# Performance work log

Hardware: AMD Instinct MI355X
Metric: run time of the kernel (lower is better)

The kernel has to match this reference:

```python
import jax, jax.numpy as jnp
import numpy as np


def setup_inputs() -> dict:
    key = jax.random.key(0)
    k1, k2, k3 = jax.random.split(key, 3)
    N, E, D_IN, D_OUT = 100000, 3200000, 256, 256
    x = jax.random.normal(k1, (N, D_IN), dtype=jnp.float32)
    W = jax.random.normal(k2, (D_OUT, D_IN), dtype=jnp.float32) * (1.0 / np.sqrt(D_IN))
    edge_index = jax.random.randint(k3, (2, E), 0, N, dtype=jnp.int32)
    return {"x": x, "W": W, "edge_index": edge_index}


def reference(x, W, edge_index):
    N = x.shape[0]
    # add self loops (static shape: E + N edges)
    loops = jnp.arange(N, dtype=edge_index.dtype)
    src = jnp.concatenate([edge_index[0], loops])  # [E+N]
    dst = jnp.concatenate([edge_index[1], loops])  # [E+N]
    # symmetric degree normalization: deg = bincount over source index
    deg = jax.ops.segment_sum(jnp.ones_like(src, dtype=x.dtype), src, num_segments=N)
    deg_rsqrt = jax.lax.rsqrt(deg)
    vals = deg_rsqrt[src] * deg_rsqrt[dst]  # [E+N]
    # dense projection then SpMM: out[i] = sum_e A[src_e=i] * h[dst_e]
    h = x @ W.T  # [N, D_OUT]
    msgs = vals[:, None] * h[dst]  # gather + scale
    out = jax.ops.segment_sum(msgs, src, num_segments=N)  # scatter-add
    return out
```

## Files before the change

kernel.cpp:

```cpp
#include <hip/hip_runtime.h>
#include <hip/hip_bf16.h>
#include <stdint.h>

#define D 256
#define NBUCK 391
#define BSHIFT 8
#define TILE 4096

typedef short short8 __attribute__((ext_vector_type(8)));
typedef float f32x4 __attribute__((ext_vector_type(4)));
typedef unsigned int u32x2 __attribute__((ext_vector_type(2)));

__device__ __forceinline__ float bf2f(unsigned short u) {
  return __uint_as_float(((unsigned)u) << 16);
}
__device__ __forceinline__ unsigned short f2bf(float f) {
  unsigned u = __float_as_uint(f);
  unsigned r = u + 0x7FFFu + ((u >> 16) & 1u);
  return (unsigned short)(r >> 16);
}

__global__ void bucket_hist_kernel(const int* __restrict__ src, int* __restrict__ bcount, int E) {
  __shared__ int h[NBUCK];
  for (int i = threadIdx.x; i < NBUCK; i += 256) h[i] = 0;
  __syncthreads();
  int gid = blockIdx.x * 256 + threadIdx.x;
  for (int e = gid; e < E; e += 256 * 256) atomicAdd(&h[src[e] >> BSHIFT], 1);
  __syncthreads();
  for (int i = threadIdx.x; i < NBUCK; i += 256) {
    int c = h[i];
    if (c) atomicAdd(&bcount[i], c);
  }
}

__global__ void bucket_scan_kernel(const int* __restrict__ bcount, int* __restrict__ bbase,
                                   int* __restrict__ gcursor) {
  __shared__ int sc[2][512];
  int tid = threadIdx.x;
  sc[0][tid] = (tid < NBUCK) ? bcount[tid] : 0;
  __syncthreads();
  int d = 0;
  for (int off = 1; off < 512; off <<= 1) {
    int v = sc[d][tid];
    if (tid >= off) v += sc[d][tid - off];
    sc[d ^ 1][tid] = v;
    __syncthreads();
    d ^= 1;
  }
  if (tid < NBUCK) {
    int excl = (tid == 0) ? 0 : sc[d][tid - 1];
    bbase[tid] = excl;
    gcursor[tid] = excl;
  }
}

__launch_bounds__(256)
__global__ void binscatter_kernel(const int* __restrict__ src, const int* __restrict__ dst,
                                  int* __restrict__ gcursor, int* __restrict__ ebuf, int E) {
  __shared__ int hist[NBUCK];
  __shared__ int lstart[512];
  __shared__ int gbase[NBUCK];
  __shared__ int sc[2][512];
  __shared__ int stag[TILE];
  __shared__ unsigned short sbuck[TILE];

  int tid = threadIdx.x;
  int base = blockIdx.x * TILE;
  int tilecount = E - base;
  if (tilecount > TILE) tilecount = TILE;

  for (int i = tid; i < NBUCK; i += 256) hist[i] = 0;
  __syncthreads();

  int esrc[16], edst[16];
#pragma unroll
  for (int k = 0; k < 16; k++) {
    int e = base + k * 256 + tid;
    if (e < E) {
      esrc[k] = src[e];
      edst[k] = dst[e];
      atomicAdd(&hist[esrc[k] >> BSHIFT], 1);
    } else {
      esrc[k] = -1;
      edst[k] = 0;
    }
  }
  __syncthreads();

  for (int i = tid; i < 512; i += 256) sc[0][i] = (i < NBUCK) ? hist[i] : 0;
  __syncthreads();
  int d = 0;
  for (int off = 1; off < 512; off <<= 1) {
    for (int i = tid; i < 512; i += 256) {
      int v = sc[d][i];
      if (i >= off) v += sc[d][i - off];
      sc[d ^ 1][i] = v;
    }
    __syncthreads();
    d ^= 1;
  }
  for (int i = tid; i < 512; i += 256) lstart[i] = (i == 0) ? 0 : sc[d][i - 1];
  __syncthreads();

  for (int b = tid; b < NBUCK; b += 256) {
    int c = hist[b];
    if (c) gbase[b] = atomicAdd(&gcursor[b], c);
  }
  __syncthreads();

  for (int i = tid; i < NBUCK; i += 256) hist[i] = 0;
  __syncthreads();

#pragma unroll
  for (int k = 0; k < 16; k++) {
    if (esrc[k] >= 0) {
      int b = esrc[k] >> BSHIFT;
      int r = atomicAdd(&hist[b], 1);
      int pos = lstart[b] + r;
      stag[pos] = edst[k] | ((esrc[k] & 255) << 20);
      sbuck[pos] = (unsigned short)b;
    }
  }
  __syncthreads();

  for (int s = tid; s < tilecount; s += 256) {
    int b = sbuck[s];
    ebuf[gbase[b] + (s - lstart[b])] = stag[s];
  }
}

__launch_bounds__(256)
__global__ void bucketsort_kernel(const int* __restrict__ ebuf, const int* __restrict__ bbase,
                                  const int* __restrict__ bcount, int* __restrict__ csr,
                                  int2* __restrict__ meta, float* __restrict__ rnorm, int N) {
  __shared__ int ncnt[256];
  __shared__ int nstart[256];
  __shared__ int sc[2][256];
  int tid = threadIdx.x;
  int b = blockIdx.x;
  int base = bbase[b];
  int cnt = bcount[b];
  int node0 = b << BSHIFT;

  ncnt[tid] = 0;
  __syncthreads();
  for (int s = tid; s < cnt; s += 256) {
    int v = ebuf[base + s];
    atomicAdd(&ncnt[v >> 20], 1);
  }
  __syncthreads();

  int mycnt = ncnt[tid];
  sc[0][tid] = mycnt;
  __syncthreads();
  int d = 0;
  for (int off = 1; off < 256; off <<= 1) {
    int v = sc[d][tid];
    if (tid >= off) v += sc[d][tid - off];
    sc[d ^ 1][tid] = v;
    __syncthreads();
    d ^= 1;
  }
  nstart[tid] = (tid == 0) ? 0 : sc[d][tid - 1];
  __syncthreads();

  int node = node0 + tid;
  if (node < N) {
    meta[node] = make_int2(base + nstart[tid], mycnt);
    rnorm[node] = rsqrtf((float)(mycnt + 1));
  }

  ncnt[tid] = 0;
  __syncthreads();
  for (int s = tid; s < cnt; s += 256) {
    int v = ebuf[base + s];
    int nl = v >> 20;
    int r = atomicAdd(&ncnt[nl], 1);
    csr[base + nstart[nl] + r] = v & 0xFFFFF;
  }
}

__global__ void convx_kernel(const float* __restrict__ x, unsigned short* __restrict__ xb,
                             int n, int npad) {
  int i4 = blockIdx.x * 256 + threadIdx.x;
  long long elem = (long long)i4 * 4;
  if (elem >= (long long)npad * D) return;
  int row = (int)(elem / D);
  ushort4 o;
  if (row < n) {
    const float4 v = *(const float4*)&x[elem];
    o.x = f2bf(v.x); o.y = f2bf(v.y); o.z = f2bf(v.z); o.w = f2bf(v.w);
  } else {
    o = make_ushort4(0, 0, 0, 0);
  }
  *(ushort4*)&xb[elem] = o;
}

__global__ void convw_kernel(const float* __restrict__ w, unsigned short* __restrict__ wb) {
  int i4 = blockIdx.x * 256 + threadIdx.x;
  int elem = i4 * 4;
  const float4 v = *(const float4*)&w[elem];
  ushort4 o;
  o.x = f2bf(v.x); o.y = f2bf(v.y); o.z = f2bf(v.z); o.w = f2bf(v.w);
  *(ushort4*)&wb[elem] = o;
}

__launch_bounds__(256)
__global__ void gemm_kernel(const unsigned short* __restrict__ A,
                            const unsigned short* __restrict__ B,
                            unsigned short* __restrict__ Hout,
                            const float* __restrict__ rnorm, int n) {
  __shared__ unsigned short sA[128 * 32];
  __shared__ unsigned short sB[128 * 32];
  int tid = threadIdx.x;
  int wave = tid >> 6, lane = tid & 63;
  int wm = wave >> 1, wn = wave & 1;
  int l16 = lane & 15, quad = lane >> 4;
  int arow0 = blockIdx.x * 128;
  int brow0 = blockIdx.y * 128;

  f32x4 acc[4][4];
  const f32x4 zero = {0.f, 0.f, 0.f, 0.f};
#pragma unroll
  for (int i = 0; i < 4; i++)
#pragma unroll
    for (int j = 0; j < 4; j++) acc[i][j] = zero;

  for (int k0 = 0; k0 < 256; k0 += 32) {
#pragma unroll
    for (int it = 0; it < 2; ++it) {
      int c = it * 256 + tid;
      int row = c >> 2, cc = (c & 3) * 8;
      *(int4*)&sA[c * 8] = *(const int4*)&A[(arow0 + row) * 256 + k0 + cc];
      *(int4*)&sB[c * 8] = *(const int4*)&B[(brow0 + row) * 256 + k0 + cc];
    }
    __syncthreads();
    short8 af[4], bfr[4];
#pragma unroll
    for (int i = 0; i < 4; i++)
      af[i] = *(const short8*)&sA[(wm * 64 + i * 16 + l16) * 32 + quad * 8];
#pragma unroll
    for (int j = 0; j < 4; j++)
      bfr[j] = *(const short8*)&sB[(wn * 64 + j * 16 + l16) * 32 + quad * 8];
#pragma unroll
    for (int i = 0; i < 4; i++)
#pragma unroll
      for (int j = 0; j < 4; j++)
        acc[i][j] = __builtin_amdgcn_mfma_f32_16x16x32_bf16(af[i], bfr[j], acc[i][j], 0, 0, 0);
    __syncthreads();
  }

#pragma unroll
  for (int i = 0; i < 4; i++) {
    int rowb = arow0 + wm * 64 + i * 16 + quad * 4;
#pragma unroll
    for (int r = 0; r < 4; r++) {
      int gr = rowb + r;
      float rn = (gr < n) ? rnorm[gr] : 0.f;
#pragma unroll
      for (int j = 0; j < 4; j++) {
        int col = brow0 + wn * 64 + j * 16 + l16;
        Hout[(size_t)gr * 256 + col] = f2bf(acc[i][j][r] * rn);
      }
    }
  }
}

__launch_bounds__(256)
__global__ void gather_kernel(const unsigned short* __restrict__ hs,
                              const int2* __restrict__ meta,
                              const float* __restrict__ rnorm,
                              const int* __restrict__ csr,
                              float* __restrict__ out, int n) {
  const int wave = threadIdx.x >> 6;
  const int lane = threadIdx.x & 63;
  const int node = blockIdx.x * 4 + wave;
  if (node >= n) return;
  long long mm = __builtin_nontemporal_load((const long long*)&meta[node]);
  const int start = (int)mm;
  const int cnt = (int)(mm >> 32);
  const int loff = lane << 2;

  float a0 = 0.f, a1 = 0.f, a2 = 0.f, a3 = 0.f;

#define GRP16(G)                                                          \
  {                                                                       \
    u32x2 v[16];                                                          \
    _Pragma("unroll")                                                     \
    for (int u = 0; u < 16; ++u) {                                        \
      int r = __builtin_amdgcn_readlane(idxv, (G) + u);                   \
      v[u] = *(const u32x2*)&hs[((size_t)r << 8) + loff];                 \
    }                                                                     \
    _Pragma("unroll")                                                     \
    for (int u = 0; u < 16; ++u) {                                        \
      a0 += bf2f((unsigned short)v[u][0]);                                \
      a1 += bf2f((unsigned short)(v[u][0] >> 16));                        \
      a2 += bf2f((unsigned short)v[u][1]);                                \
      a3 += bf2f((unsigned short)(v[u][1] >> 16));                        \
    }                                                                     \
  }

  int idxv = __builtin_nontemporal_load(&csr[start + lane]);
  int base = 0;
  while (base + 64 <= cnt) {
    int idxn = __builtin_nontemporal_load(&csr[start + base + 64 + lane]);
    GRP16(0) GRP16(16) GRP16(32) GRP16(48)
    idxv = idxn;
    base += 64;
  }
  int m = cnt - base;
  int g = 0;
  for (; g + 16 <= m; g += 16) GRP16(g)
  for (; g < m; ++g) {
    int r = __builtin_amdgcn_readlane(idxv, g);
    u32x2 v = *(const u32x2*)&hs[((size_t)r << 8) + loff];
    a0 += bf2f((unsigned short)v[0]);
    a1 += bf2f((unsigned short)(v[0] >> 16));
    a2 += bf2f((unsigned short)v[1]);
    a3 += bf2f((unsigned short)(v[1] >> 16));
  }
#undef GRP16

  u32x2 us = *(const u32x2*)&hs[((size_t)node << 8) + loff];
  float rn = __builtin_nontemporal_load(&rnorm[node]);
  f32x4 o;
  o[0] = rn * (a0 + bf2f((unsigned short)us[0]));
  o[1] = rn * (a1 + bf2f((unsigned short)(us[0] >> 16)));
  o[2] = rn * (a2 + bf2f((unsigned short)us[1]));
  o[3] = rn * (a3 + bf2f((unsigned short)(us[1] >> 16)));
  __builtin_nontemporal_store(o, (f32x4*)&out[(size_t)node * 256 + loff]);
}

extern "C" void kernel_launch(void* const* d_in, const int* in_sizes, int n_in,
                              void* d_out, int out_size, void* d_ws, size_t ws_size,
                              hipStream_t stream) {
  const float* x = (const float*)d_in[0];
  const float* W = (const float*)d_in[1];
  const int* ei = (const int*)d_in[2];
  float* out = (float*)d_out;

  int N = in_sizes[0] / D;
  int E = in_sizes[2] / 2;
  int NPAD = (N + 127) & ~127;
  const int* src = ei;
  const int* dst = ei + E;

  char* p = (char*)d_ws;
  auto alloc = [&](size_t b) {
    char* r = p;
    p += (b + 255) & ~(size_t)255;
    return r;
  };
  unsigned short* xb = (unsigned short*)alloc((size_t)NPAD * D * 2);
  unsigned short* wb = (unsigned short*)alloc((size_t)D * D * 2);
  unsigned short* hb = (unsigned short*)alloc((size_t)NPAD * D * 2);
  int* csr = (int*)alloc((size_t)(E + 64) * 4);
  int2* meta = (int2*)alloc((size_t)N * 8);
  float* rnorm = (float*)alloc((size_t)N * 4);
  int* bcount = (int*)alloc(NBUCK * 4);
  int* bbase = (int*)alloc(NBUCK * 4);
  int* gcursor = (int*)alloc(NBUCK * 4);
  int* ebuf = (int*)hb;

  hipMemsetAsync(bcount, 0, NBUCK * 4, stream);
  bucket_hist_kernel<<<256, 256, 0, stream>>>(src, bcount, E);
  bucket_scan_kernel<<<1, 512, 0, stream>>>(bcount, bbase, gcursor);
  binscatter_kernel<<<(E + TILE - 1) / TILE, 256, 0, stream>>>(src, dst, gcursor, ebuf, E);
  bucketsort_kernel<<<NBUCK, 256, 0, stream>>>(ebuf, bbase, bcount, csr, meta, rnorm, N);
  convx_kernel<<<(NPAD * (D / 4) + 255) / 256, 256, 0, stream>>>(x, xb, N, NPAD);
  convw_kernel<<<(D * D / 4) / 256, 256, 0, stream>>>(W, wb);
  gemm_kernel<<<dim3(NPAD / 128, D / 128), 256, 0, stream>>>(xb, wb, hb, rnorm, N);
  gather_kernel<<<(N + 3) / 4, 256, 0, stream>>>(hb, meta, rnorm, csr, out, N);
}
```

Baseline: 548.2 us.

## Fuse fp32-to-bf16 conversion of x into GEMM and widen tile to full N

Removes the separate convx kernel and converts x from fp32 to bf16 while loading it into shared memory inside the GEMM. Each block now computes all 256 output columns, so each x row is read once instead of twice. This saves a full pass writing and rereading the bf16 copy of x. In exchange it doubles the accumulator registers per thread (128 floats) and the B tile in shared memory, which can lower occupancy and the overlap of global loads with compute.

```diff
diff --git a/kernel.cpp b/kernel.cpp
--- a/kernel.cpp
+++ b/kernel.cpp
@@ -180,22 +180,6 @@
   }
 }
 
-__global__ void convx_kernel(const float* __restrict__ x, unsigned short* __restrict__ xb,
-                             int n, int npad) {
-  int i4 = blockIdx.x * 256 + threadIdx.x;
-  long long elem = (long long)i4 * 4;
-  if (elem >= (long long)npad * D) return;
-  int row = (int)(elem / D);
-  ushort4 o;
-  if (row < n) {
-    const float4 v = *(const float4*)&x[elem];
-    o.x = f2bf(v.x); o.y = f2bf(v.y); o.z = f2bf(v.z); o.w = f2bf(v.w);
-  } else {
-    o = make_ushort4(0, 0, 0, 0);
-  }
-  *(ushort4*)&xb[elem] = o;
-}
-
 __global__ void convw_kernel(const float* __restrict__ w, unsigned short* __restrict__ wb) {
   int i4 = blockIdx.x * 256 + threadIdx.x;
   int elem = i4 * 4;
@@ -206,46 +190,59 @@
 }
 
 __launch_bounds__(256)
-__global__ void gemm_kernel(const unsigned short* __restrict__ A,
+__global__ void gemm_kernel(const float* __restrict__ X,
                             const unsigned short* __restrict__ B,
                             unsigned short* __restrict__ Hout,
                             const float* __restrict__ rnorm, int n) {
   __shared__ unsigned short sA[128 * 32];
-  __shared__ unsigned short sB[128 * 32];
+  __shared__ unsigned short sB[256 * 32];
   int tid = threadIdx.x;
   int wave = tid >> 6, lane = tid & 63;
   int wm = wave >> 1, wn = wave & 1;
   int l16 = lane & 15, quad = lane >> 4;
   int arow0 = blockIdx.x * 128;
-  int brow0 = blockIdx.y * 128;
-
-  f32x4 acc[4][4];
+
+  f32x4 acc[4][8];
   const f32x4 zero = {0.f, 0.f, 0.f, 0.f};
 #pragma unroll
   for (int i = 0; i < 4; i++)
 #pragma unroll
-    for (int j = 0; j < 4; j++) acc[i][j] = zero;
+    for (int j = 0; j < 8; j++) acc[i][j] = zero;
 
   for (int k0 = 0; k0 < 256; k0 += 32) {
 #pragma unroll
     for (int it = 0; it < 2; ++it) {
       int c = it * 256 + tid;
       int row = c >> 2, cc = (c & 3) * 8;
-      *(int4*)&sA[c * 8] = *(const int4*)&A[(arow0 + row) * 256 + k0 + cc];
-      *(int4*)&sB[c * 8] = *(const int4*)&B[(brow0 + row) * 256 + k0 + cc];
-    }
-    __syncthreads();
-    short8 af[4], bfr[4];
+      int grow = arow0 + row;
+      ushort4 lo = make_ushort4(0, 0, 0, 0), hi = make_ushort4(0, 0, 0, 0);
+      if (grow < n) {
+        const float4 v0 = *(const float4*)&X[(size_t)grow * 256 + k0 + cc];
+        const float4 v1 = *(const float4*)&X[(size_t)grow * 256 + k0 + cc + 4];
+        lo.x = f2bf(v0.x); lo.y = f2bf(v0.y); lo.z = f2bf(v0.z); lo.w = f2bf(v0.w);
+        hi.x = f2bf(v1.x); hi.y = f2bf(v1.y); hi.z = f2bf(v1.z); hi.w = f2bf(v1.w);
+      }
+      *(ushort4*)&sA[c * 8] = lo;
+      *(ushort4*)&sA[c * 8 + 4] = hi;
+    }
+#pragma unroll
+    for (int it = 0; it < 4; ++it) {
+      int c = it * 256 + tid;
+      int row = c >> 2, cc = (c & 3) * 8;
+      *(int4*)&sB[c * 8] = *(const int4*)&B[row * 256 + k0 + cc];
+    }
+    __syncthreads();
+    short8 af[4], bfr[8];
 #pragma unroll
     for (int i = 0; i < 4; i++)
       af[i] = *(const short8*)&sA[(wm * 64 + i * 16 + l16) * 32 + quad * 8];
 #pragma unroll
-    for (int j = 0; j < 4; j++)
-      bfr[j] = *(const short8*)&sB[(wn * 64 + j * 16 + l16) * 32 + quad * 8];
+    for (int j = 0; j < 8; j++)
+      bfr[j] = *(const short8*)&sB[(wn * 128 + j * 16 + l16) * 32 + quad * 8];
 #pragma unroll
     for (int i = 0; i < 4; i++)
 #pragma unroll
-      for (int j = 0; j < 4; j++)
+      for (int j = 0; j < 8; j++)
         acc[i][j] = __builtin_amdgcn_mfma_f32_16x16x32_bf16(af[i], bfr[j], acc[i][j], 0, 0, 0);
     __syncthreads();
   }
@@ -258,8 +255,8 @@
       int gr = rowb + r;
       float rn = (gr < n) ? rnorm[gr] : 0.f;
 #pragma unroll
-      for (int j = 0; j < 4; j++) {
-        int col = brow0 + wn * 64 + j * 16 + l16;
+      for (int j = 0; j < 8; j++) {
+        int col = wn * 128 + j * 16 + l16;
         Hout[(size_t)gr * 256 + col] = f2bf(acc[i][j][r] * rn);
       }
     }
@@ -351,7 +348,6 @@
     p += (b + 255) & ~(size_t)255;
     return r;
   };
-  unsigned short* xb = (unsigned short*)alloc((size_t)NPAD * D * 2);
   unsigned short* wb = (unsigned short*)alloc((size_t)D * D * 2);
   unsigned short* hb = (unsigned short*)alloc((size_t)NPAD * D * 2);
   int* csr = (int*)alloc((size_t)(E + 64) * 4);
@@ -367,8 +363,7 @@
   bucket_scan_kernel<<<1, 512, 0, stream>>>(bcount, bbase, gcursor);
   binscatter_kernel<<<(E + TILE - 1) / TILE, 256, 0, stream>>>(src, dst, gcursor, ebuf, E);
   bucketsort_kernel<<<NBUCK, 256, 0, stream>>>(ebuf, bbase, bcount, csr, meta, rnorm, N);
-  convx_kernel<<<(NPAD * (D / 4) + 255) / 256, 256, 0, stream>>>(x, xb, N, NPAD);
   convw_kernel<<<(D * D / 4) / 256, 256, 0, stream>>>(W, wb);
-  gemm_kernel<<<dim3(NPAD / 128, D / 128), 256, 0, stream>>>(xb, wb, hb, rnorm, N);
+  gemm_kernel<<<NPAD / 128, 256, 0, stream>>>(x, wb, hb, rnorm, N);
   gather_kernel<<<(N + 3) / 4, 256, 0, stream>>>(hb, meta, rnorm, csr, out, N);
 }
```

After: 568.2 us. 1.04x slower.

## Replace two-level bucket sort CSR build with per-node atomic counting sort

Applied to the files above, without the earlier changes.

Replaces the bucketed two-pass CSR construction (bucket histogram, bin scatter through LDS, per-bucket local sort) with a direct counting sort: global per-node atomic counts, a two-level block scan, then a scatter that uses per-node global atomic cursors. This removes the intermediate ebuf pass and the LDS staging. In exchange it relies on millions of scattered global atomics and random csr writes. Edge order within each row becomes nondeterministic, which changes the float summation order.

```diff
diff --git a/kernel.cpp b/kernel.cpp
--- a/kernel.cpp
+++ b/kernel.cpp
@@ -3,9 +3,6 @@
 #include <stdint.h>
 
 #define D 256
-#define NBUCK 391
-#define BSHIFT 8
-#define TILE 4096
 
 typedef short short8 __attribute__((ext_vector_type(8)));
 typedef float f32x4 __attribute__((ext_vector_type(4)));
@@ -20,163 +17,72 @@
   return (unsigned short)(r >> 16);
 }
 
-__global__ void bucket_hist_kernel(const int* __restrict__ src, int* __restrict__ bcount, int E) {
-  __shared__ int h[NBUCK];
-  for (int i = threadIdx.x; i < NBUCK; i += 256) h[i] = 0;
-  __syncthreads();
+__global__ void count_kernel(const int* __restrict__ src, int* __restrict__ ecount, int E) {
   int gid = blockIdx.x * 256 + threadIdx.x;
-  for (int e = gid; e < E; e += 256 * 256) atomicAdd(&h[src[e] >> BSHIFT], 1);
-  __syncthreads();
-  for (int i = threadIdx.x; i < NBUCK; i += 256) {
-    int c = h[i];
-    if (c) atomicAdd(&bcount[i], c);
-  }
-}
-
-__global__ void bucket_scan_kernel(const int* __restrict__ bcount, int* __restrict__ bbase,
-                                   int* __restrict__ gcursor) {
-  __shared__ int sc[2][512];
+  int stride = gridDim.x * 256;
+  for (int e = gid; e < E; e += stride) atomicAdd(&ecount[src[e]], 1);
+}
+
+__launch_bounds__(1024)
+__global__ void scan1_kernel(const int* __restrict__ ecount, int* __restrict__ offloc,
+                             int* __restrict__ btot, int N) {
+  __shared__ int sc[2][1024];
   int tid = threadIdx.x;
-  sc[0][tid] = (tid < NBUCK) ? bcount[tid] : 0;
+  int node = blockIdx.x * 1024 + tid;
+  int v = (node < N) ? ecount[node] : 0;
+  sc[0][tid] = v;
   __syncthreads();
   int d = 0;
-  for (int off = 1; off < 512; off <<= 1) {
-    int v = sc[d][tid];
-    if (tid >= off) v += sc[d][tid - off];
-    sc[d ^ 1][tid] = v;
+  for (int off = 1; off < 1024; off <<= 1) {
+    int x = sc[d][tid];
+    if (tid >= off) x += sc[d][tid - off];
+    sc[d ^ 1][tid] = x;
     __syncthreads();
     d ^= 1;
   }
-  if (tid < NBUCK) {
-    int excl = (tid == 0) ? 0 : sc[d][tid - 1];
-    bbase[tid] = excl;
-    gcursor[tid] = excl;
-  }
-}
-
-__launch_bounds__(256)
-__global__ void binscatter_kernel(const int* __restrict__ src, const int* __restrict__ dst,
-                                  int* __restrict__ gcursor, int* __restrict__ ebuf, int E) {
-  __shared__ int hist[NBUCK];
-  __shared__ int lstart[512];
-  __shared__ int gbase[NBUCK];
-  __shared__ int sc[2][512];
-  __shared__ int stag[TILE];
-  __shared__ unsigned short sbuck[TILE];
-
+  if (node < N) offloc[node] = sc[d][tid] - v;
+  if (tid == 1023) btot[blockIdx.x] = sc[d][1023];
+}
+
+__launch_bounds__(1024)
+__global__ void finalize_kernel(const int* __restrict__ ecount, const int* __restrict__ offloc,
+                                const int* __restrict__ btot, int nb,
+                                int2* __restrict__ meta, float* __restrict__ rnorm,
+                                int* __restrict__ cursor, int N) {
+  __shared__ int sb[2][128];
   int tid = threadIdx.x;
-  int base = blockIdx.x * TILE;
-  int tilecount = E - base;
-  if (tilecount > TILE) tilecount = TILE;
-
-  for (int i = tid; i < NBUCK; i += 256) hist[i] = 0;
-  __syncthreads();
-
-  int esrc[16], edst[16];
-#pragma unroll
-  for (int k = 0; k < 16; k++) {
-    int e = base + k * 256 + tid;
-    if (e < E) {
-      esrc[k] = src[e];
-      edst[k] = dst[e];
-      atomicAdd(&hist[esrc[k] >> BSHIFT], 1);
-    } else {
-      esrc[k] = -1;
-      edst[k] = 0;
-    }
-  }
-  __syncthreads();
-
-  for (int i = tid; i < 512; i += 256) sc[0][i] = (i < NBUCK) ? hist[i] : 0;
+  if (tid < 128) sb[0][tid] = (tid < nb) ? btot[tid] : 0;
   __syncthreads();
   int d = 0;
-  for (int off = 1; off < 512; off <<= 1) {
-    for (int i = tid; i < 512; i += 256) {
-      int v = sc[d][i];
-      if (i >= off) v += sc[d][i - off];
-      sc[d ^ 1][i] = v;
+  for (int off = 1; off < 128; off <<= 1) {
+    if (tid < 128) {
+      int x = sb[d][tid];
+      if (tid >= off) x += sb[d][tid - off];
+      sb[d ^ 1][tid] = x;
     }
     __syncthreads();
     d ^= 1;
   }
-  for (int i = tid; i < 512; i += 256) lstart[i] = (i == 0) ? 0 : sc[d][i - 1];
-  __syncthreads();
-
-  for (int b = tid; b < NBUCK; b += 256) {
-    int c = hist[b];
-    if (c) gbase[b] = atomicAdd(&gcursor[b], c);
-  }
-  __syncthreads();
-
-  for (int i = tid; i < NBUCK; i += 256) hist[i] = 0;
-  __syncthreads();
-
-#pragma unroll
-  for (int k = 0; k < 16; k++) {
-    if (esrc[k] >= 0) {
-      int b = esrc[k] >> BSHIFT;
-      int r = atomicAdd(&hist[b], 1);
-      int pos = lstart[b] + r;
-      stag[pos] = edst[k] | ((esrc[k] & 255) << 20);
-      sbuck[pos] = (unsigned short)b;
-    }
-  }
-  __syncthreads();
-
-  for (int s = tid; s < tilecount; s += 256) {
-    int b = sbuck[s];
-    ebuf[gbase[b] + (s - lstart[b])] = stag[s];
-  }
-}
-
-__launch_bounds__(256)
-__global__ void bucketsort_kernel(const int* __restrict__ ebuf, const int* __restrict__ bbase,
-                                  const int* __restrict__ bcount, int* __restrict__ csr,
-                                  int2* __restrict__ meta, float* __restrict__ rnorm, int N) {
-  __shared__ int ncnt[256];
-  __shared__ int nstart[256];
-  __shared__ int sc[2][256];
-  int tid = threadIdx.x;
   int b = blockIdx.x;
-  int base = bbase[b];
-  int cnt = bcount[b];
-  int node0 = b << BSHIFT;
-
-  ncnt[tid] = 0;
-  __syncthreads();
-  for (int s = tid; s < cnt; s += 256) {
-    int v = ebuf[base + s];
-    atomicAdd(&ncnt[v >> 20], 1);
-  }
-  __syncthreads();
-
-  int mycnt = ncnt[tid];
-  sc[0][tid] = mycnt;
-  __syncthreads();
-  int d = 0;
-  for (int off = 1; off < 256; off <<= 1) {
-    int v = sc[d][tid];
-    if (tid >= off) v += sc[d][tid - off];
-    sc[d ^ 1][tid] = v;
-    __syncthreads();
-    d ^= 1;
-  }
-  nstart[tid] = (tid == 0) ? 0 : sc[d][tid - 1];
-  __syncthreads();
-
-  int node = node0 + tid;
+  int base = (b == 0) ? 0 : sb[d][b - 1];
+  int node = b * 1024 + tid;
   if (node < N) {
-    meta[node] = make_int2(base + nstart[tid], mycnt);
-    rnorm[node] = rsqrtf((float)(mycnt + 1));
-  }
-
-  ncnt[tid] = 0;
-  __syncthreads();
-  for (int s = tid; s < cnt; s += 256) {
-    int v = ebuf[base + s];
-    int nl = v >> 20;
-    int r = atomicAdd(&ncnt[nl], 1);
-    csr[base + nstart[nl] + r] = v & 0xFFFFF;
+    int cnt = ecount[node];
+    int off = base + offloc[node];
+    meta[node] = make_int2(off, cnt);
+    cursor[node] = off;
+    rnorm[node] = rsqrtf((float)(cnt + 1));
+  }
+}
+
+__global__ void scatter_kernel(const int* __restrict__ src, const int* __restrict__ dst,
+                               int* __restrict__ cursor, int* __restrict__ csr, int E) {
+  int gid = blockIdx.x * 256 + threadIdx.x;
+  int stride = gridDim.x * 256;
+  for (int e = gid; e < E; e += stride) {
+    int s = src[e];
+    int pos = atomicAdd(&cursor[s], 1);
+    csr[pos] = dst[e];
   }
 }
 
@@ -342,6 +248,7 @@
   int N = in_sizes[0] / D;
   int E = in_sizes[2] / 2;
   int NPAD = (N + 127) & ~127;
+  int NB = (N + 1023) / 1024;
   const int* src = ei;
   const int* dst = ei + E;
 
@@ -357,16 +264,16 @@
   int* csr = (int*)alloc((size_t)(E + 64) * 4);
   int2* meta = (int2*)alloc((size_t)N * 8);
   float* rnorm = (float*)alloc((size_t)N * 4);
-  int* bcount = (int*)alloc(NBUCK * 4);
-  int* bbase = (int*)alloc(NBUCK * 4);
-  int* gcursor = (int*)alloc(NBUCK * 4);
-  int* ebuf = (int*)hb;
-
-  hipMemsetAsync(bcount, 0, NBUCK * 4, stream);
-  bucket_hist_kernel<<<256, 256, 0, stream>>>(src, bcount, E);
-  bucket_scan_kernel<<<1, 512, 0, stream>>>(bcount, bbase, gcursor);
-  binscatter_kernel<<<(E + TILE - 1) / TILE, 256, 0, stream>>>(src, dst, gcursor, ebuf, E);
-  bucketsort_kernel<<<NBUCK, 256, 0, stream>>>(ebuf, bbase, bcount, csr, meta, rnorm, N);
+  int* ecount = (int*)alloc((size_t)N * 4);
+  int* offloc = (int*)alloc((size_t)N * 4);
+  int* cursor = (int*)alloc((size_t)N * 4);
+  int* btot = (int*)alloc(128 * 4);
+
+  hipMemsetAsync(ecount, 0, (size_t)N * 4, stream);
+  count_kernel<<<2048, 256, 0, stream>>>(src, ecount, E);
+  scan1_kernel<<<NB, 1024, 0, stream>>>(ecount, offloc, btot, N);
+  finalize_kernel<<<NB, 1024, 0, stream>>>(ecount, offloc, btot, NB, meta, rnorm, cursor, N);
+  scatter_kernel<<<2048, 256, 0, stream>>>(src, dst, cursor, csr, E);
   convx_kernel<<<(NPAD * (D / 4) + 255) / 256, 256, 0, stream>>>(x, xb, N, NPAD);
   convw_kernel<<<(D * D / 4) / 256, 256, 0, stream>>>(W, wb);
   gemm_kernel<<<dim3(NPAD / 128, D / 128), 256, 0, stream>>>(xb, wb, hb, rnorm, N);
```

After: 859.1 us. 1.57x slower.
